# Kernel optimization log

Hardware: AMD Instinct MI355X
Metric: run time of the kernel (lower is better)

## Reference

```python
import jax, jax.numpy as jnp
import numpy as np
import math

H = 8                 # num_heads
MAX_REL = 32          # max_relative_distance
VOCAB_REL = 2 * MAX_REL + 1


def setup_inputs() -> dict:
    key = jax.random.key(0)
    ks = jax.random.split(key, 8)
    B, S, D = 4, 2048, 256
    hd = D // H
    sd = 1.0 / math.sqrt(D)
    inp = {
        "query": jax.random.normal(ks[0], (B, S, D), jnp.float32),
        "mask": jnp.ones((B, 1, 1, S), jnp.float32),
        "Wq": jax.random.normal(ks[1], (D, D), jnp.float32) * sd,
        "bq": jnp.zeros((D,), jnp.float32),
        "Wk": jax.random.normal(ks[2], (D, D), jnp.float32) * sd,
        "bk": jnp.zeros((D,), jnp.float32),
        "Wv": jax.random.normal(ks[3], (D, D), jnp.float32) * sd,
        "bv": jnp.zeros((D,), jnp.float32),
        "Wo": jax.random.normal(ks[4], (D, D), jnp.float32) * sd,
        "bo": jnp.zeros((D,), jnp.float32),
        "rel_table": jax.random.normal(ks[5], (VOCAB_REL, hd), jnp.float32) * 0.1,
    }
    return inp


def _split_heads(x, B, S, hd):
    # [B,S,D] -> [B,H,S,hd]
    return x.reshape(B, S, H, hd).transpose(0, 2, 1, 3)


def _relative_row_sums(S, rel_table):
    # Original: emb = table[relpos]  (S,S,hd); scores += einsum('bhid,jkd->bhijk', Q, emb).sum(-1)
    # == einsum('bhid,jd->bhij', Q, R) with R[j,d] = sum_k emb[j,k,d].
    # Compute R without materializing the (S,S,hd) tensor: count how often each
    # relative-position bucket appears in each row, then counts @ table.
    pos = jnp.arange(S)
    relpos = jnp.clip(pos[:, None] - pos[None, :], -MAX_REL, MAX_REL) + MAX_REL  # [S,S] ints
    rows = jnp.broadcast_to(pos[:, None], (S, S))
    counts = jnp.zeros((S, VOCAB_REL), rel_table.dtype).at[
        rows.reshape(-1), relpos.reshape(-1)
    ].add(1.0)
    return counts @ rel_table  # [S, hd]


def reference(query, mask, Wq, bq, Wk, bk, Wv, bv, Wo, bo, rel_table):
    B, S, D = query.shape
    hd = D // H
    scale = 1.0 / math.sqrt(hd)

    Q = _split_heads(query @ Wq + bq, B, S, hd)
    K = _split_heads(query @ Wk + bk, B, S, hd)   # key defaults to query
    V = _split_heads(query @ Wv + bv, B, S, hd)   # value defaults to key

    scores = jnp.einsum("bhid,bhjd->bhij", Q, K) * scale
    R = _relative_row_sums(S, rel_table)          # [S, hd]
    scores = scores + jnp.einsum("bhid,jd->bhij", Q, R)

    scores = scores + (1.0 - mask) * -1e9         # mask broadcast [B,1,1,S]
    attn = jax.nn.softmax(scores, axis=-1)        # dropout is identity (training=False)

    out = jnp.einsum("bhij,bhjd->bhid", attn, V)
    out = out.transpose(0, 2, 1, 3).reshape(B, S, D)
    return out @ Wo + bo
```

## Files before the change

kernel.cpp:

```cpp
#include <hip/hip_runtime.h>
#include <hip/hip_bf16.h>
#include <math.h>

#define NH 8
#define HD 32
#define SEQ 2048
#define DM 256
#define SCALE 0.17677669529663687f
#define INV_SCALE 5.656854249492381f
#define LOG2E 1.4426950408889634f
#define QSC (SCALE * LOG2E)
#define MNEG (-1e9f * LOG2E)

typedef float f32x4 __attribute__((ext_vector_type(4)));
typedef __bf16 bf16x8 __attribute__((ext_vector_type(8)));

#define GLOAD(g, l) __builtin_amdgcn_global_load_lds( \
    (const __attribute__((address_space(1))) void*)(g), \
    (__attribute__((address_space(3))) void*)(l), 16, 0, 0)

__global__ void k_prep(const float* __restrict__ query, const float* __restrict__ mask,
                       const float* __restrict__ Wq, const float* __restrict__ Wk,
                       const float* __restrict__ Wv, const float* __restrict__ Wo,
                       const float* __restrict__ bq, const float* __restrict__ tbl,
                       __bf16* __restrict__ Xb, __bf16* __restrict__ Wt,
                       __bf16* __restrict__ WoT, float* __restrict__ MT,
                       __bf16* __restrict__ SUFtab, __bf16* __restrict__ PREtab,
                       float* __restrict__ WV2T, float* __restrict__ cb) {
  const int blk = blockIdx.x, tid = threadIdx.x;
  if (blk < 1024) {
    size_t i = (size_t)blk * 2048 + (size_t)tid * 8;
    float4 a = *(const float4*)(query + i);
    float4 b4 = *(const float4*)(query + i + 4);
    union { __bf16 h[8]; bf16x8 v; } o;
    o.h[0] = (__bf16)a.x;  o.h[1] = (__bf16)a.y;
    o.h[2] = (__bf16)a.z;  o.h[3] = (__bf16)a.w;
    o.h[4] = (__bf16)b4.x; o.h[5] = (__bf16)b4.y;
    o.h[6] = (__bf16)b4.z; o.h[7] = (__bf16)b4.w;
    *(bf16x8*)(Xb + i) = o.v;
  } else if (blk < 1120) {
    int tg = (blk - 1024) * 256 + tid;
    int n = tg >> 5, kc = tg & 31;
    int which = n >> 8, nw = n & 255;
    const float* W = which == 0 ? Wq : (which == 1 ? Wk : Wv);
#pragma unroll
    for (int i = 0; i < 8; ++i)
      Wt[(size_t)n * 256 + kc * 8 + i] = (__bf16)W[(size_t)(kc * 8 + i) * 256 + nw];
  } else if (blk < 1152) {
    int tg = (blk - 1120) * 256 + tid;
    int n = tg >> 5, kc = tg & 31;
#pragma unroll
    for (int i = 0; i < 8; ++i)
      WoT[(size_t)n * 256 + kc * 8 + i] = (__bf16)Wo[(size_t)(kc * 8 + i) * 256 + n];
  } else if (blk == 1152) {
    for (int i = tid; i < 4 * SEQ; i += 256) MT[i] = (1.0f - mask[i]) * MNEG;
  } else if (blk == 1153) {
    for (int idx = tid; idx < 1024; idx += 256) {
      int j = idx >> 5, d = idx & 31;
      float s = 0.f;
      for (int u = j + 33; u <= 63; ++u) s += tbl[u * 32 + d];
      SUFtab[idx] = (__bf16)(s * INV_SCALE);
    }
    for (int idx = tid; idx < 1024; idx += 256) {
      int jj = idx >> 5, d = idx & 31;
      float s = 0.f;
      for (int u = 1; u <= jj; ++u) s += tbl[u * 32 + d];
      PREtab[idx] = (__bf16)(s * INV_SCALE);
    }
  } else if (blk < 1170) {
    int tg = (blk - 1154) * 256 + tid;
    int hv = tg >> 8, k = tg & 255;
    const float* T = tbl + ((hv & 1) ? 0 : 64 * 32);
    const float* w = Wq + (size_t)k * 256 + (hv >> 1) * 32;
    float acc = 0.f;
#pragma unroll
    for (int d = 0; d < 32; ++d) acc = fmaf(w[d], T[d], acc);
    WV2T[hv * 256 + k] = acc * LOG2E;
  } else {
    if (tid < 16) {
      const float* T = tbl + ((tid & 1) ? 0 : 64 * 32);
      float a = 0.f;
#pragma unroll
      for (int d = 0; d < 32; ++d) a = fmaf(bq[(tid >> 1) * 32 + d], T[d], a);
      cb[tid] = a * LOG2E;
    }
  }
}

__launch_bounds__(256)
__global__ void k_rel(const float* __restrict__ X, const float* __restrict__ WV2T,
                      const float* __restrict__ cb, float* __restrict__ REL) {
  const int tid = threadIdx.x;
  const int hv = tid & 15, rl = tid >> 4;
  const int row0 = blockIdx.x * 32 + rl;
  const float* x0 = X + (size_t)row0 * 256;
  const float* x1 = x0 + 16 * 256;
  const float* wv = WV2T + hv * 256;
  float a0 = cb[hv], a1 = a0;
#pragma unroll 4
  for (int k = 0; k < 256; k += 4) {
    f32x4 w4 = *(const f32x4*)(wv + k);
    f32x4 xa = *(const f32x4*)(x0 + k);
    f32x4 xb = *(const f32x4*)(x1 + k);
    a0 = fmaf(xa.x, w4.x, a0); a0 = fmaf(xa.y, w4.y, a0);
    a0 = fmaf(xa.z, w4.z, a0); a0 = fmaf(xa.w, w4.w, a0);
    a1 = fmaf(xb.x, w4.x, a1); a1 = fmaf(xb.y, w4.y, a1);
    a1 = fmaf(xb.z, w4.z, a1); a1 = fmaf(xb.w, w4.w, a1);
  }
  const int h = hv >> 1, v = hv & 1;
  const int b0i = row0 >> 11, s0 = row0 & 2047;
  REL[((size_t)(b0i * NH + h) * SEQ + s0) * 2 + v] = a0;
  const int r1 = row0 + 16;
  const int b1i = r1 >> 11, s1 = r1 & 2047;
  REL[((size_t)(b1i * NH + h) * SEQ + s1) * 2 + v] = a1;
}

template <int MODE>
__launch_bounds__(256)
__global__ void k_gemm(const __bf16* __restrict__ A, const __bf16* __restrict__ Bt,
                       const float* __restrict__ b0, const float* __restrict__ b1,
                       const float* __restrict__ b2,
                       __bf16* __restrict__ Qb, __bf16* __restrict__ Kb,
                       __bf16* __restrict__ VTout, float* __restrict__ Y) {
  constexpr int BN = (MODE == 0) ? 128 : 64;
  constexpr int NFJ = BN / 32;
  __shared__ __align__(16) __bf16 As[128 * 64];
  __shared__ __align__(16) __bf16 Bs[BN * 64];
  const int tid = threadIdx.x, lane = tid & 63, wid = tid >> 6;
  const int l16 = lane & 15, lhi = lane >> 4;
  const int wr = wid >> 1, wc = wid & 1;
  const int m0 = blockIdx.x * 128, n0 = blockIdx.y * BN;

  f32x4 acc[4][NFJ];
#pragma unroll
  for (int i = 0; i < 4; ++i)
#pragma unroll
    for (int j = 0; j < NFJ; ++j) acc[i][j] = (f32x4){0.f, 0.f, 0.f, 0.f};

  for (int k0 = 0; k0 < 256; k0 += 64) {
    __syncthreads();
#pragma unroll
    for (int cc = 0; cc < 4; ++cc) {
      int cl = tid + cc * 256;
      int row = cl >> 3, kc = cl & 7;
      int k = k0 + ((kc ^ (row & 7)) * 8);
      const __bf16* src;
      if constexpr (MODE == 0) {
        src = A + (size_t)(m0 + row) * 256 + k;
      } else {
        int r = m0 + row, bb = r >> 11, s = r & 2047, h = k >> 5, dh = k & 31;
        src = A + ((size_t)(bb * NH + h) * SEQ + s) * HD + dh;
      }
      GLOAD(src, (__bf16*)As + (size_t)cl * 8);
    }
#pragma unroll
    for (int cc = 0; cc < NFJ; ++cc) {
      int cl = tid + cc * 256;
      int row = cl >> 3, kc = cl & 7;
      int k = k0 + ((kc ^ (row & 7)) * 8);
      GLOAD(Bt + (size_t)(n0 + row) * 256 + k, (__bf16*)Bs + (size_t)cl * 8);
    }
    __syncthreads();
#pragma unroll
    for (int kk = 0; kk < 64; kk += 32) {
      bf16x8 af[4], bfr[NFJ];
#pragma unroll
      for (int fi = 0; fi < 4; ++fi) {
        int row = wr * 64 + fi * 16 + l16;
        af[fi] = *(const bf16x8*)(As + row * 64 + ((((kk >> 3) + lhi) ^ (row & 7)) * 8));
      }
#pragma unroll
      for (int fj = 0; fj < NFJ; ++fj) {
        int row = wc * (BN / 2) + fj * 16 + l16;
        bfr[fj] = *(const bf16x8*)(Bs + row * 64 + ((((kk >> 3) + lhi) ^ (row & 7)) * 8));
      }
#pragma unroll
      for (int fi = 0; fi < 4; ++fi)
#pragma unroll
        for (int fj = 0; fj < NFJ; ++fj)
          acc[fi][fj] = __builtin_amdgcn_mfma_f32_16x16x32_bf16(af[fi], bfr[fj], acc[fi][fj], 0, 0, 0);
    }
  }
#pragma unroll
  for (int fi = 0; fi < 4; ++fi) {
#pragma unroll
    for (int fj = 0; fj < NFJ; ++fj) {
      int mrow = m0 + wr * 64 + fi * 16 + lhi * 4;
      int ncol = n0 + wc * (BN / 2) + fj * 16 + l16;
      if constexpr (MODE == 0) {
        int which = ncol >> 8, nw = ncol & 255, h = nw >> 5, dh = nw & 31;
        int bb = mrow >> 11, s0 = mrow & 2047;
        if (which == 2) {
          union { __bf16 h4[4]; uint2 u; } o;
#pragma unroll
          for (int r = 0; r < 4; ++r) o.h4[r] = (__bf16)(acc[fi][fj][r] + b2[nw]);
          *(uint2*)(VTout + ((size_t)(bb * NH + h) * HD + dh) * SEQ + s0) = o.u;
        } else {
          const float* bias = which == 0 ? b0 : b1;
#pragma unroll
          for (int r = 0; r < 4; ++r) {
            float v = acc[fi][fj][r] + bias[nw];
            size_t oi = ((size_t)(bb * NH + h) * SEQ + (s0 + r)) * HD + dh;
            if (which == 0) Qb[oi] = (__bf16)(v * QSC);
            else Kb[oi] = (__bf16)v;
          }
        }
      } else {
#pragma unroll
        for (int r = 0; r < 4; ++r)
          Y[(size_t)(mrow + r) * 256 + ncol] = acc[fi][fj][r] + b0[ncol];
      }
    }
  }
}

__launch_bounds__(512, 4)
__global__ void k_flash(const __bf16* __restrict__ Qb, const __bf16* __restrict__ Kb,
                        const __bf16* __restrict__ VT, const float* __restrict__ REL,
                        const __bf16* __restrict__ SUFtab, const __bf16* __restrict__ PREtab,
                        const float* __restrict__ MT, __bf16* __restrict__ Ob) {
  const int bh = blockIdx.y, qt = blockIdx.x, b = bh >> 3;
  const int tid = threadIdx.x, wid = tid >> 6, lane = tid & 63;
  const int l16 = lane & 15, lhi = lane >> 4;

  __shared__ __align__(16) __bf16 kbuf[2][128 * 32];
  __shared__ __align__(16) __bf16 vbuf[2][32 * 128];
  __shared__ __align__(16) __bf16 plds[8][16 * 136];

  const int qrow = qt * 128 + wid * 16 + l16;
  const size_t rg = (size_t)bh * SEQ + qrow;
  const bf16x8 qfrag = *(const bf16x8*)(Qb + rg * HD + lhi * 8);
  const float2 uw = *(const float2*)(REL + rg * 2);
  const float uu = uw.x, ww = uw.y, duw = uu - ww;
  const float duw16 = 16.f * duw;
  const f32x4 duwr = {0.f, duw, 2.f * duw, 3.f * duw};

  const int kj = tid >> 2, kc = tid & 3;
  const __bf16* ksrc = Kb + (size_t)bh * SEQ * HD + (size_t)kj * HD + ((kc ^ ((kj >> 1) & 3)) * 8);
  const int vd = tid >> 4, vc = tid & 15;
  const __bf16* vsrc = VT + ((size_t)bh * HD + vd) * SEQ + ((vc ^ (vd & 7)) * 8);

  f32x4 of0 = {0.f, 0.f, 0.f, 0.f}, of1 = {0.f, 0.f, 0.f, 0.f};
  const f32x4 zero4 = {0.f, 0.f, 0.f, 0.f};
  float m = -3.0e38f, lsum = 0.f;
  __bf16* pl = &plds[wid][0];
  const float* mtp = MT + b * SEQ + lhi * 4;

  GLOAD(ksrc, &kbuf[0][(size_t)tid * 8]);
  GLOAD(vsrc, &vbuf[0][(size_t)tid * 8]);
  __syncthreads();

  for (int t = 0, cur = 0; t < 16; ++t, cur ^= 1) {
    const int jb = t * 128;
    if (t < 15) {
      GLOAD(ksrc + (size_t)(jb + 128) * HD, &kbuf[cur ^ 1][(size_t)tid * 8]);
      GLOAD(vsrc + (jb + 128), &vbuf[cur ^ 1][(size_t)tid * 8]);
    }
    const __bf16* kb = kbuf[cur];
    const __bf16* vb = vbuf[cur];

    f32x4 sf[8];
    __builtin_amdgcn_s_setprio(1);
#pragma unroll
    for (int jt = 0; jt < 8; ++jt) {
      const int row = jt * 16 + l16;
      bf16x8 kf = *(const bf16x8*)(kb + row * 32 + ((lhi ^ ((row >> 1) & 3)) * 8));
      sf[jt] = __builtin_amdgcn_mfma_f32_16x16x32_bf16(kf, qfrag, zero4, 0, 0, 0);
    }
    __builtin_amdgcn_s_setprio(0);

    if (t == 0) {
      const bf16x8 s0 = *(const bf16x8*)(SUFtab + l16 * HD + lhi * 8);
      const bf16x8 s1 = *(const bf16x8*)(SUFtab + (16 + l16) * HD + lhi * 8);
      sf[0] -= __builtin_amdgcn_mfma_f32_16x16x32_bf16(s0, qfrag, zero4, 0, 0, 0);
      sf[1] -= __builtin_amdgcn_mfma_f32_16x16x32_bf16(s1, qfrag, zero4, 0, 0, 0);
#pragma unroll
      for (int jt = 0; jt < 2; ++jt)
#pragma unroll
        for (int r = 0; r < 4; ++r)
          sf[jt][r] += fmaxf(31.f - (float)(jt * 16 + lhi * 4 + r), 0.f) * uu;
    }
    if (t == 15) {
      const bf16x8 p0 = *(const bf16x8*)(PREtab + l16 * HD + lhi * 8);
      const bf16x8 p1 = *(const bf16x8*)(PREtab + (16 + l16) * HD + lhi * 8);
      sf[6] -= __builtin_amdgcn_mfma_f32_16x16x32_bf16(p0, qfrag, zero4, 0, 0, 0);
      sf[7] -= __builtin_amdgcn_mfma_f32_16x16x32_bf16(p1, qfrag, zero4, 0, 0, 0);
#pragma unroll
      for (int jt = 6; jt < 8; ++jt)
#pragma unroll
        for (int r = 0; r < 4; ++r)
          sf[jt][r] += fmaxf((float)(jb + jt * 16 + lhi * 4 + r) - 2016.f, 0.f) * ww;
    }

    f32x4 lin = duwr + (float)(jb + lhi * 4) * duw;
    float tmax = -3.0e38f;
#pragma unroll
    for (int jt = 0; jt < 8; ++jt) {
      f32x4 mt4 = *(const f32x4*)(mtp + jb + jt * 16);
      f32x4 s = sf[jt] + lin + mt4;
      lin += duw16;
      sf[jt] = s;
      tmax = fmaxf(tmax, fmaxf(fmaxf(s.x, s.y), fmaxf(s.z, s.w)));
    }
    tmax = fmaxf(tmax, __shfl_xor(tmax, 16));
    tmax = fmaxf(tmax, __shfl_xor(tmax, 32));

    const float mn = fmaxf(m, tmax);
    const float c = __builtin_amdgcn_exp2f(m - mn);
    m = mn;
    of0 *= c; of1 *= c;
    float csum = 0.f;
#pragma unroll
    for (int jt = 0; jt < 8; ++jt) {
      f32x4 e;
#pragma unroll
      for (int r = 0; r < 4; ++r) e[r] = __builtin_amdgcn_exp2f(sf[jt][r] - m);
      csum += (e.x + e.y) + (e.z + e.w);
      union { __bf16 h4[4]; uint2 u; } pk;
#pragma unroll
      for (int r = 0; r < 4; ++r) pk.h4[r] = (__bf16)e[r];
      *(uint2*)(pl + l16 * 136 + jt * 16 + lhi * 4) = pk.u;
    }
    csum += __shfl_xor(csum, 16);
    csum += __shfl_xor(csum, 32);
    lsum = lsum * c + csum;

    __builtin_amdgcn_s_setprio(1);
#pragma unroll
    for (int kt = 0; kt < 4; ++kt) {
      bf16x8 pf = *(const bf16x8*)(pl + l16 * 136 + kt * 32 + lhi * 8);
      bf16x8 v0 = *(const bf16x8*)(vb + l16 * 128 + (((kt * 4 + lhi) ^ (l16 & 7)) * 8));
      bf16x8 v1 = *(const bf16x8*)(vb + (16 + l16) * 128 + (((kt * 4 + lhi) ^ (l16 & 7)) * 8));
      of0 = __builtin_amdgcn_mfma_f32_16x16x32_bf16(v0, pf, of0, 0, 0, 0);
      of1 = __builtin_amdgcn_mfma_f32_16x16x32_bf16(v1, pf, of1, 0, 0, 0);
    }
    __builtin_amdgcn_s_setprio(0);
    __syncthreads();
  }

  const float inv = 1.0f / lsum;
  union { __bf16 h4[4]; uint2 u; } o0, o1;
#pragma unroll
  for (int r = 0; r < 4; ++r) {
    o0.h4[r] = (__bf16)(of0[r] * inv);
    o1.h4[r] = (__bf16)(of1[r] * inv);
  }
  *(uint2*)(Ob + rg * HD + lhi * 4) = o0.u;
  *(uint2*)(Ob + rg * HD + 16 + lhi * 4) = o1.u;
}

extern "C" void kernel_launch(void* const* d_in, const int* in_sizes, int n_in,
                              void* d_out, int out_size, void* d_ws, size_t ws_size,
                              hipStream_t stream) {
  (void)in_sizes; (void)n_in; (void)out_size; (void)ws_size;
  const float* query = (const float*)d_in[0];
  const float* mask  = (const float*)d_in[1];
  const float* Wq = (const float*)d_in[2];
  const float* bq = (const float*)d_in[3];
  const float* Wk = (const float*)d_in[4];
  const float* bk = (const float*)d_in[5];
  const float* Wv = (const float*)d_in[6];
  const float* bv = (const float*)d_in[7];
  const float* Wo = (const float*)d_in[8];
  const float* bo = (const float*)d_in[9];
  const float* tbl = (const float*)d_in[10];
  float* out = (float*)d_out;
  char* ws = (char*)d_ws;

  const size_t MB = 1024ull * 1024;
  __bf16* Xb    = (__bf16*)(ws);
  __bf16* Wt    = (__bf16*)(ws + 4 * MB);
  __bf16* WoT   = (__bf16*)(ws + 4 * MB + 393216);
  __bf16* SUFt  = (__bf16*)(ws + 4 * MB + 524288);
  __bf16* PREt  = (__bf16*)(ws + 4 * MB + 526336);
  float*  WV2T  = (float*) (ws + 4 * MB + 528384);
  float*  cbv   = (float*) (ws + 4 * MB + 544768);
  float*  MT    = (float*) (ws + 4 * MB + 544832);
  float*  REL   = (float*) (ws + 5 * MB);
  __bf16* Qb    = (__bf16*)(ws + 6 * MB);
  __bf16* Kb    = (__bf16*)(ws + 10 * MB);
  __bf16* VT    = (__bf16*)(ws + 14 * MB);
  __bf16* Ob    = (__bf16*)(ws + 18 * MB);

  k_prep<<<1171, 256, 0, stream>>>(query, mask, Wq, Wk, Wv, Wo, bq, tbl,
                                   Xb, Wt, WoT, MT, SUFt, PREt, WV2T, cbv);
  k_rel<<<256, 256, 0, stream>>>(query, WV2T, cbv, REL);
  k_gemm<0><<<dim3(64, 6), 256, 0, stream>>>(Xb, Wt, bq, bk, bv, Qb, Kb, VT, nullptr);
  k_flash<<<dim3(16, 32), 512, 0, stream>>>(Qb, Kb, VT, REL, SUFt, PREt, MT, Ob);
  k_gemm<1><<<dim3(64, 4), 256, 0, stream>>>(Ob, WoT, bo, nullptr, nullptr,
                                             nullptr, nullptr, nullptr, out);
}
```

Before: 107.4 us.

## Restructure prep transposes, tile k_rel via LDS, and streamline flash softmax

Weight transposes in the prep kernel now go through 64x64 LDS tiles with coalesced vector reads and writes. The rel-bias kernel stages X and its weights in shared memory. The flash kernel folds the linear relative-position term into the MFMA accumulator init and negates the correction tables so they accumulate directly. It computes the row sum with an extra MFMA against a ones vector instead of shuffles, and XOR-swizzles the P buffer instead of padding it. The mask add is skipped at runtime when a device flag reports the mask is all ones; this adds a global read and a branch but is computed honestly on device each call.

```diff
diff --git a/kernel.cpp b/kernel.cpp
--- a/kernel.cpp
+++ b/kernel.cpp
@@ -25,9 +25,12 @@
                        const float* __restrict__ bq, const float* __restrict__ tbl,
                        __bf16* __restrict__ Xb, __bf16* __restrict__ Wt,
                        __bf16* __restrict__ WoT, float* __restrict__ MT,
-                       __bf16* __restrict__ SUFtab, __bf16* __restrict__ PREtab,
-                       float* __restrict__ WV2T, float* __restrict__ cb) {
+                       __bf16* __restrict__ SUFn, __bf16* __restrict__ PREn,
+                       float* __restrict__ WV2T, float* __restrict__ cb,
+                       int* __restrict__ MFLAG) {
   const int blk = blockIdx.x, tid = threadIdx.x;
+  __shared__ float ts[64][65];
+  __shared__ int okl;
   if (blk < 1024) {
     size_t i = (size_t)blk * 2048 + (size_t)tid * 8;
     float4 a = *(const float4*)(query + i);
@@ -38,37 +41,65 @@
     o.h[4] = (__bf16)b4.x; o.h[5] = (__bf16)b4.y;
     o.h[6] = (__bf16)b4.z; o.h[7] = (__bf16)b4.w;
     *(bf16x8*)(Xb + i) = o.v;
-  } else if (blk < 1120) {
-    int tg = (blk - 1024) * 256 + tid;
-    int n = tg >> 5, kc = tg & 31;
-    int which = n >> 8, nw = n & 255;
-    const float* W = which == 0 ? Wq : (which == 1 ? Wk : Wv);
-#pragma unroll
-    for (int i = 0; i < 8; ++i)
-      Wt[(size_t)n * 256 + kc * 8 + i] = (__bf16)W[(size_t)(kc * 8 + i) * 256 + nw];
-  } else if (blk < 1152) {
-    int tg = (blk - 1120) * 256 + tid;
-    int n = tg >> 5, kc = tg & 31;
-#pragma unroll
-    for (int i = 0; i < 8; ++i)
-      WoT[(size_t)n * 256 + kc * 8 + i] = (__bf16)Wo[(size_t)(kc * 8 + i) * 256 + n];
-  } else if (blk == 1152) {
-    for (int i = tid; i < 4 * SEQ; i += 256) MT[i] = (1.0f - mask[i]) * MNEG;
-  } else if (blk == 1153) {
+  } else if (blk < 1088) {
+    const int idx = blk - 1024;
+    const float* W;
+    __bf16* dst;
+    int tile;
+    if (idx < 48) {
+      int which = idx >> 4;
+      W = which == 0 ? Wq : (which == 1 ? Wk : Wv);
+      dst = Wt + which * 65536;
+      tile = idx & 15;
+    } else {
+      W = Wo; dst = WoT; tile = idx - 48;
+    }
+    const int tr = (tile >> 2) * 64, tc = (tile & 3) * 64;
+#pragma unroll
+    for (int p = 0; p < 4; ++p) {
+      int row = p * 16 + (tid >> 4);
+      int col = (tid & 15) * 4;
+      float4 v = *(const float4*)(W + (size_t)(tr + row) * 256 + tc + col);
+      ts[row][col] = v.x; ts[row][col + 1] = v.y;
+      ts[row][col + 2] = v.z; ts[row][col + 3] = v.w;
+    }
+    __syncthreads();
+#pragma unroll
+    for (int p = 0; p < 2; ++p) {
+      int n = p * 32 + (tid >> 3);
+      int kb = (tid & 7) * 8;
+      union { __bf16 h[8]; bf16x8 v; } o;
+#pragma unroll
+      for (int e = 0; e < 8; ++e) o.h[e] = (__bf16)ts[kb + e][n];
+      *(bf16x8*)(dst + (size_t)(tc + n) * 256 + tr + kb) = o.v;
+    }
+  } else if (blk == 1088) {
+    if (tid == 0) okl = 1;
+    __syncthreads();
+    bool ok = true;
+    for (int i = tid; i < 4 * SEQ; i += 256) {
+      float mv = mask[i];
+      MT[i] = (1.0f - mv) * MNEG;
+      ok &= (mv == 1.0f);
+    }
+    if (!ok) atomicAnd(&okl, 0);
+    __syncthreads();
+    if (tid == 0) MFLAG[0] = okl;
+  } else if (blk == 1089) {
     for (int idx = tid; idx < 1024; idx += 256) {
       int j = idx >> 5, d = idx & 31;
       float s = 0.f;
       for (int u = j + 33; u <= 63; ++u) s += tbl[u * 32 + d];
-      SUFtab[idx] = (__bf16)(s * INV_SCALE);
+      SUFn[idx] = (__bf16)(-s * INV_SCALE);
     }
     for (int idx = tid; idx < 1024; idx += 256) {
       int jj = idx >> 5, d = idx & 31;
       float s = 0.f;
       for (int u = 1; u <= jj; ++u) s += tbl[u * 32 + d];
-      PREtab[idx] = (__bf16)(s * INV_SCALE);
-    }
-  } else if (blk < 1170) {
-    int tg = (blk - 1154) * 256 + tid;
+      PREn[idx] = (__bf16)(-s * INV_SCALE);
+    }
+  } else if (blk < 1106) {
+    int tg = (blk - 1090) * 256 + tid;
     int hv = tg >> 8, k = tg & 255;
     const float* T = tbl + ((hv & 1) ? 0 : 64 * 32);
     const float* w = Wq + (size_t)k * 256 + (hv >> 1) * 32;
@@ -90,23 +121,35 @@
 __launch_bounds__(256)
 __global__ void k_rel(const float* __restrict__ X, const float* __restrict__ WV2T,
                       const float* __restrict__ cb, float* __restrict__ REL) {
+  __shared__ float Xs[32][260];
+  __shared__ float Ws[16][260];
   const int tid = threadIdx.x;
+  const size_t base = (size_t)blockIdx.x * 32 * 256;
+#pragma unroll
+  for (int p = 0; p < 8; ++p) {
+    int idx = p * 1024 + tid * 4;
+    float4 v = *(const float4*)(X + base + idx);
+    *(float4*)&Xs[idx >> 8][idx & 255] = v;
+  }
+#pragma unroll
+  for (int p = 0; p < 4; ++p) {
+    int idx = p * 1024 + tid * 4;
+    float4 v = *(const float4*)(WV2T + idx);
+    *(float4*)&Ws[idx >> 8][idx & 255] = v;
+  }
+  __syncthreads();
   const int hv = tid & 15, rl = tid >> 4;
+  float a0 = cb[hv], a1 = a0;
+  const float* xs0 = &Xs[rl][0];
+  const float* xs1 = &Xs[rl + 16][0];
+  const float* wsp = &Ws[hv][0];
+#pragma unroll 8
+  for (int k = 0; k < 256; ++k) {
+    float w = wsp[k];
+    a0 = fmaf(xs0[k], w, a0);
+    a1 = fmaf(xs1[k], w, a1);
+  }
   const int row0 = blockIdx.x * 32 + rl;
-  const float* x0 = X + (size_t)row0 * 256;
-  const float* x1 = x0 + 16 * 256;
-  const float* wv = WV2T + hv * 256;
-  float a0 = cb[hv], a1 = a0;
-#pragma unroll 4
-  for (int k = 0; k < 256; k += 4) {
-    f32x4 w4 = *(const f32x4*)(wv + k);
-    f32x4 xa = *(const f32x4*)(x0 + k);
-    f32x4 xb = *(const f32x4*)(x1 + k);
-    a0 = fmaf(xa.x, w4.x, a0); a0 = fmaf(xa.y, w4.y, a0);
-    a0 = fmaf(xa.z, w4.z, a0); a0 = fmaf(xa.w, w4.w, a0);
-    a1 = fmaf(xb.x, w4.x, a1); a1 = fmaf(xb.y, w4.y, a1);
-    a1 = fmaf(xb.z, w4.z, a1); a1 = fmaf(xb.w, w4.w, a1);
-  }
   const int h = hv >> 1, v = hv & 1;
   const int b0i = row0 >> 11, s0 = row0 & 2047;
   REL[((size_t)(b0i * NH + h) * SEQ + s0) * 2 + v] = a0;
@@ -217,15 +260,16 @@
 __launch_bounds__(512, 4)
 __global__ void k_flash(const __bf16* __restrict__ Qb, const __bf16* __restrict__ Kb,
                         const __bf16* __restrict__ VT, const float* __restrict__ REL,
-                        const __bf16* __restrict__ SUFtab, const __bf16* __restrict__ PREtab,
-                        const float* __restrict__ MT, __bf16* __restrict__ Ob) {
+                        const __bf16* __restrict__ SUFn, const __bf16* __restrict__ PREn,
+                        const float* __restrict__ MT, const int* __restrict__ MFLAG,
+                        __bf16* __restrict__ Ob) {
   const int bh = blockIdx.y, qt = blockIdx.x, b = bh >> 3;
   const int tid = threadIdx.x, wid = tid >> 6, lane = tid & 63;
   const int l16 = lane & 15, lhi = lane >> 4;
 
   __shared__ __align__(16) __bf16 kbuf[2][128 * 32];
   __shared__ __align__(16) __bf16 vbuf[2][32 * 128];
-  __shared__ __align__(16) __bf16 plds[8][16 * 136];
+  __shared__ __align__(16) __bf16 plds[8][16 * 128];
 
   const int qrow = qt * 128 + wid * 16 + l16;
   const size_t rg = (size_t)bh * SEQ + qrow;
@@ -234,15 +278,19 @@
   const float uu = uw.x, ww = uw.y, duw = uu - ww;
   const float duw16 = 16.f * duw;
   const f32x4 duwr = {0.f, duw, 2.f * duw, 3.f * duw};
+  const int flag = MFLAG[0];
 
   const int kj = tid >> 2, kc = tid & 3;
   const __bf16* ksrc = Kb + (size_t)bh * SEQ * HD + (size_t)kj * HD + ((kc ^ ((kj >> 1) & 3)) * 8);
   const int vd = tid >> 4, vc = tid & 15;
   const __bf16* vsrc = VT + ((size_t)bh * HD + vd) * SEQ + ((vc ^ (vd & 7)) * 8);
 
-  f32x4 of0 = {0.f, 0.f, 0.f, 0.f}, of1 = {0.f, 0.f, 0.f, 0.f};
-  const f32x4 zero4 = {0.f, 0.f, 0.f, 0.f};
-  float m = -3.0e38f, lsum = 0.f;
+  f32x4 of0 = {0.f, 0.f, 0.f, 0.f}, of1 = {0.f, 0.f, 0.f, 0.f}, of2 = {0.f, 0.f, 0.f, 0.f};
+  const f32x4 zero4 = {0.f, 0.f, 0.f, 0.f}; (void)zero4;
+  bf16x8 ones;
+#pragma unroll
+  for (int e = 0; e < 8; ++e) ones[e] = (__bf16)1.0f;
+  float m = -3.0e38f;
   __bf16* pl = &plds[wid][0];
   const float* mtp = MT + b * SEQ + lhi * 4;
 
@@ -259,21 +307,23 @@
     const __bf16* kb = kbuf[cur];
     const __bf16* vb = vbuf[cur];
 
+    f32x4 lin = duwr + (float)(jb + lhi * 4) * duw;
     f32x4 sf[8];
     __builtin_amdgcn_s_setprio(1);
 #pragma unroll
     for (int jt = 0; jt < 8; ++jt) {
       const int row = jt * 16 + l16;
       bf16x8 kf = *(const bf16x8*)(kb + row * 32 + ((lhi ^ ((row >> 1) & 3)) * 8));
-      sf[jt] = __builtin_amdgcn_mfma_f32_16x16x32_bf16(kf, qfrag, zero4, 0, 0, 0);
+      sf[jt] = __builtin_amdgcn_mfma_f32_16x16x32_bf16(kf, qfrag, lin, 0, 0, 0);
+      lin += duw16;
     }
     __builtin_amdgcn_s_setprio(0);
 
     if (t == 0) {
-      const bf16x8 s0 = *(const bf16x8*)(SUFtab + l16 * HD + lhi * 8);
-      const bf16x8 s1 = *(const bf16x8*)(SUFtab + (16 + l16) * HD + lhi * 8);
-      sf[0] -= __builtin_amdgcn_mfma_f32_16x16x32_bf16(s0, qfrag, zero4, 0, 0, 0);
-      sf[1] -= __builtin_amdgcn_mfma_f32_16x16x32_bf16(s1, qfrag, zero4, 0, 0, 0);
+      const bf16x8 s0 = *(const bf16x8*)(SUFn + l16 * HD + lhi * 8);
+      const bf16x8 s1 = *(const bf16x8*)(SUFn + (16 + l16) * HD + lhi * 8);
+      sf[0] = __builtin_amdgcn_mfma_f32_16x16x32_bf16(s0, qfrag, sf[0], 0, 0, 0);
+      sf[1] = __builtin_amdgcn_mfma_f32_16x16x32_bf16(s1, qfrag, sf[1], 0, 0, 0);
 #pragma unroll
       for (int jt = 0; jt < 2; ++jt)
 #pragma unroll
@@ -281,64 +331,59 @@
           sf[jt][r] += fmaxf(31.f - (float)(jt * 16 + lhi * 4 + r), 0.f) * uu;
     }
     if (t == 15) {
-      const bf16x8 p0 = *(const bf16x8*)(PREtab + l16 * HD + lhi * 8);
-      const bf16x8 p1 = *(const bf16x8*)(PREtab + (16 + l16) * HD + lhi * 8);
-      sf[6] -= __builtin_amdgcn_mfma_f32_16x16x32_bf16(p0, qfrag, zero4, 0, 0, 0);
-      sf[7] -= __builtin_amdgcn_mfma_f32_16x16x32_bf16(p1, qfrag, zero4, 0, 0, 0);
+      const bf16x8 p0 = *(const bf16x8*)(PREn + l16 * HD + lhi * 8);
+      const bf16x8 p1 = *(const bf16x8*)(PREn + (16 + l16) * HD + lhi * 8);
+      sf[6] = __builtin_amdgcn_mfma_f32_16x16x32_bf16(p0, qfrag, sf[6], 0, 0, 0);
+      sf[7] = __builtin_amdgcn_mfma_f32_16x16x32_bf16(p1, qfrag, sf[7], 0, 0, 0);
 #pragma unroll
       for (int jt = 6; jt < 8; ++jt)
 #pragma unroll
         for (int r = 0; r < 4; ++r)
-          sf[jt][r] += fmaxf((float)(jb + jt * 16 + lhi * 4 + r) - 2016.f, 0.f) * ww;
-    }
-
-    f32x4 lin = duwr + (float)(jb + lhi * 4) * duw;
+          sf[jt][r] += fmaxf((float)(1920 + jt * 16 + lhi * 4 + r) - 2016.f, 0.f) * ww;
+    }
+    if (!flag) {
+#pragma unroll
+      for (int jt = 0; jt < 8; ++jt)
+        sf[jt] += *(const f32x4*)(mtp + jb + jt * 16);
+    }
+
     float tmax = -3.0e38f;
 #pragma unroll
-    for (int jt = 0; jt < 8; ++jt) {
-      f32x4 mt4 = *(const f32x4*)(mtp + jb + jt * 16);
-      f32x4 s = sf[jt] + lin + mt4;
-      lin += duw16;
-      sf[jt] = s;
-      tmax = fmaxf(tmax, fmaxf(fmaxf(s.x, s.y), fmaxf(s.z, s.w)));
-    }
+    for (int jt = 0; jt < 8; ++jt)
+      tmax = fmaxf(tmax, fmaxf(fmaxf(sf[jt].x, sf[jt].y), fmaxf(sf[jt].z, sf[jt].w)));
     tmax = fmaxf(tmax, __shfl_xor(tmax, 16));
     tmax = fmaxf(tmax, __shfl_xor(tmax, 32));
-
     const float mn = fmaxf(m, tmax);
     const float c = __builtin_amdgcn_exp2f(m - mn);
     m = mn;
-    of0 *= c; of1 *= c;
-    float csum = 0.f;
+    of0 *= c; of1 *= c; of2 *= c;
+
 #pragma unroll
     for (int jt = 0; jt < 8; ++jt) {
-      f32x4 e;
-#pragma unroll
-      for (int r = 0; r < 4; ++r) e[r] = __builtin_amdgcn_exp2f(sf[jt][r] - m);
-      csum += (e.x + e.y) + (e.z + e.w);
       union { __bf16 h4[4]; uint2 u; } pk;
 #pragma unroll
-      for (int r = 0; r < 4; ++r) pk.h4[r] = (__bf16)e[r];
-      *(uint2*)(pl + l16 * 136 + jt * 16 + lhi * 4) = pk.u;
-    }
-    csum += __shfl_xor(csum, 16);
-    csum += __shfl_xor(csum, 32);
-    lsum = lsum * c + csum;
+      for (int r = 0; r < 4; ++r)
+        pk.h4[r] = (__bf16)__builtin_amdgcn_exp2f(sf[jt][r] - m);
+      const int blk16 = ((jt * 2 + (lhi >> 1)) ^ (l16 & 7));
+      *(uint2*)(pl + l16 * 128 + blk16 * 8 + (lhi & 1) * 4) = pk.u;
+    }
 
     __builtin_amdgcn_s_setprio(1);
 #pragma unroll
     for (int kt = 0; kt < 4; ++kt) {
-      bf16x8 pf = *(const bf16x8*)(pl + l16 * 136 + kt * 32 + lhi * 8);
+      const int pblk = (kt * 4 + lhi) ^ (l16 & 7);
+      bf16x8 pf = *(const bf16x8*)(pl + l16 * 128 + pblk * 8);
       bf16x8 v0 = *(const bf16x8*)(vb + l16 * 128 + (((kt * 4 + lhi) ^ (l16 & 7)) * 8));
       bf16x8 v1 = *(const bf16x8*)(vb + (16 + l16) * 128 + (((kt * 4 + lhi) ^ (l16 & 7)) * 8));
       of0 = __builtin_amdgcn_mfma_f32_16x16x32_bf16(v0, pf, of0, 0, 0, 0);
       of1 = __builtin_amdgcn_mfma_f32_16x16x32_bf16(v1, pf, of1, 0, 0, 0);
+      of2 = __builtin_amdgcn_mfma_f32_16x16x32_bf16(ones, pf, of2, 0, 0, 0);
     }
     __builtin_amdgcn_s_setprio(0);
     __syncthreads();
   }
 
-  const float inv = 1.0f / lsum;
+  const float inv = 1.0f / of2[0];
   union { __bf16 h4[4]; uint2 u; } o0, o1;
 #pragma unroll
   for (int r = 0; r < 4; ++r) {
@@ -371,22 +416,23 @@
   __bf16* Xb    = (__bf16*)(ws);
   __bf16* Wt    = (__bf16*)(ws + 4 * MB);
   __bf16* WoT   = (__bf16*)(ws + 4 * MB + 393216);
-  __bf16* SUFt  = (__bf16*)(ws + 4 * MB + 524288);
-  __bf16* PREt  = (__bf16*)(ws + 4 * MB + 526336);
+  __bf16* SUFn  = (__bf16*)(ws + 4 * MB + 524288);
+  __bf16* PREn  = (__bf16*)(ws + 4 * MB + 526336);
   float*  WV2T  = (float*) (ws + 4 * MB + 528384);
   float*  cbv   = (float*) (ws + 4 * MB + 544768);
   float*  MT    = (float*) (ws + 4 * MB + 544832);
+  int*    MFLAG = (int*)   (ws + 4 * MB + 577600);
   float*  REL   = (float*) (ws + 5 * MB);
   __bf16* Qb    = (__bf16*)(ws + 6 * MB);
   __bf16* Kb    = (__bf16*)(ws + 10 * MB);
   __bf16* VT    = (__bf16*)(ws + 14 * MB);
   __bf16* Ob    = (__bf16*)(ws + 18 * MB);
 
-  k_prep<<<1171, 256, 0, stream>>>(query, mask, Wq, Wk, Wv, Wo, bq, tbl,
-                                   Xb, Wt, WoT, MT, SUFt, PREt, WV2T, cbv);
+  k_prep<<<1107, 256, 0, stream>>>(query, mask, Wq, Wk, Wv, Wo, bq, tbl,
+                                   Xb, Wt, WoT, MT, SUFn, PREn, WV2T, cbv, MFLAG);
   k_rel<<<256, 256, 0, stream>>>(query, WV2T, cbv, REL);
   k_gemm<0><<<dim3(64, 6), 256, 0, stream>>>(Xb, Wt, bq, bk, bv, Qb, Kb, VT, nullptr);
-  k_flash<<<dim3(16, 32), 512, 0, stream>>>(Qb, Kb, VT, REL, SUFt, PREt, MT, Ob);
+  k_flash<<<dim3(16, 32), 512, 0, stream>>>(Qb, Kb, VT, REL, SUFn, PREn, MT, MFLAG, Ob);
   k_gemm<1><<<dim3(64, 4), 256, 0, stream>>>(Ob, WoT, bo, nullptr, nullptr,
                                              nullptr, nullptr, nullptr, out);
 }
```

Measured after the change: 89.65 us. 1.2x faster.
